# Optimization experiments

Measured on AMD Instinct MI355X. Metric: run time of the kernel, lower is better.

The kernel has to match this reference:

```python
import jax, jax.numpy as jnp
import numpy as np

D = 1024
H = 4 * D
E = 8
K = 2


def setup_inputs() -> dict:
    key = jax.random.key(0)
    ks = jax.random.split(key, 8)
    s = 1.0 / np.sqrt(D)
    sh = 1.0 / np.sqrt(H)
    return {
        "x": jax.random.normal(ks[0], (4, 2048, D), dtype=jnp.float32),
        "gate_w": jax.random.uniform(ks[1], (D, E), jnp.float32, -s, s),
        "gate_b": jax.random.uniform(ks[2], (E,), jnp.float32, -s, s),
        "w1": jax.random.uniform(ks[3], (E, D, H), jnp.float32, -s, s),
        "b1": jax.random.uniform(ks[4], (E, H), jnp.float32, -s, s),
        "w2": jax.random.uniform(ks[5], (E, H, D), jnp.float32, -sh, sh),
        "b2": jax.random.uniform(ks[6], (E, D), jnp.float32, -sh, sh),
    }


def reference(x, gate_w, gate_b, w1, b1, w2, b2):
    # Gating: softmax over experts, top-k, renormalize.
    gate_logits = jnp.einsum("bsd,de->bse", x, gate_w) + gate_b
    weights = jax.nn.softmax(gate_logits, axis=-1)
    top_w, top_idx = jax.lax.top_k(weights, K)  # [B,S,K]
    top_w = top_w / jnp.sum(top_w, axis=-1, keepdims=True)

    out = jnp.zeros_like(x)
    # Loop over the fixed, small set of experts; dense FFN per expert,
    # masked-weighted combine (same math as the per-token torch loop).
    for e in range(E):
        # combine weight for expert e per token: sum of top_w where selected
        w_e = jnp.sum(jnp.where(top_idx == e, top_w, 0.0), axis=-1)  # [B,S]
        h = jax.nn.gelu(jnp.einsum("bsd,dh->bsh", x, w1[e]) + b1[e], approximate=False)
        y = jnp.einsum("bsh,hd->bsd", h, w2[e]) + b2[e]
        out = out + w_e[..., None] * y
    return out
```

## Files before the change

### kernel.cpp

```cpp
#include <hip/hip_runtime.h>
#include <math.h>

#define T_TOK 8192
#define DDIM  1024
#define HDIM  4096
#define NEXP  8
#define BM    128
#define BN    128
#define BK    64
#define MAXROWS (T_TOK*2 + NEXP*BM)
#define MAXTILES (MAXROWS/BM)
#define KS2   2
#define NGATE (T_TOK/8)
#define NTR1  ((HDIM/64)*(DDIM/64)*NEXP)
#define NTR2  ((DDIM/64)*(HDIM/64)*NEXP)

typedef __attribute__((ext_vector_type(8))) short short8;
typedef __attribute__((ext_vector_type(4))) short short4v;
typedef __attribute__((ext_vector_type(4))) float f32x4;

typedef const __attribute__((address_space(1))) unsigned int* gp1_t;
typedef __attribute__((address_space(3))) unsigned int* lp3_t;

__device__ __forceinline__ void gld16(const void* g, void* l) {
  __builtin_amdgcn_global_load_lds((gp1_t)g, (lp3_t)l, 16, 0, 0);
}

__device__ __forceinline__ short f2bf(float f) {
  unsigned u = __float_as_uint(f);
  u += 0x7fffu + ((u >> 16) & 1u);
  return (short)(u >> 16);
}

__device__ __forceinline__ float erf_fast(float x) {
  float ax = fabsf(x);
  float t = 1.f / (1.f + 0.3275911f * ax);
  float poly = t * (0.254829592f + t * (-0.284496736f + t * (1.421413741f +
               t * (-1.453152027f + t * 1.061405429f))));
  float r = 1.f - poly * __expf(-ax * ax);
  return copysignf(r, x);
}

__device__ __forceinline__ void tr_body(float* sl ,
    const float* __restrict__ w, short* __restrict__ wt, int R, int C, int lb) {
  int ctiles = C / 64, rtiles = R / 64;
  int e  = lb / (ctiles * rtiles);
  int rm = lb % (ctiles * rtiles);
  int r0 = (rm / ctiles) * 64;
  int c0 = (rm % ctiles) * 64;
  const float* W = w + (size_t)e * R * C;
  short* O = wt + (size_t)e * R * C;
  int t = threadIdx.x;
  int lr = t >> 4, lc4 = (t & 15) * 4;
#pragma unroll
  for (int i = 0; i < 4; i++) {
    float4 v = *(const float4*)&W[(size_t)(r0 + lr + i * 16) * C + c0 + lc4];
    sl[(lr + i * 16) * 65 + lc4 + 0] = v.x;
    sl[(lr + i * 16) * 65 + lc4 + 1] = v.y;
    sl[(lr + i * 16) * 65 + lc4 + 2] = v.z;
    sl[(lr + i * 16) * 65 + lc4 + 3] = v.w;
  }
  __syncthreads();
#pragma unroll
  for (int i = 0; i < 4; i++) {
    int oc = lr + i * 16;
    short4v s;
#pragma unroll
    for (int j = 0; j < 4; j++) s[j] = f2bf(sl[(lc4 + j) * 65 + oc]);
    *(short4v*)&O[(size_t)(c0 + oc) * R + r0 + lc4] = s;
  }
}

__device__ __forceinline__ void gate_body(char* smem, int bid,
    const float* __restrict__ x, const float* __restrict__ gw,
    const float* __restrict__ gb, int2* __restrict__ toke,
    float2* __restrict__ tokw, int* __restrict__ bcnt, short* __restrict__ xb) {
  float* sg = (float*)smem;
  int* lcnt = (int*)(smem + NEXP * DDIM * 4);
  int t = threadIdx.x;
#pragma unroll
  for (int it = 0; it < 8; ++it) {
    int l0 = (it * 256 + t) * 4;
    float4 v = *(const float4*)&gw[l0];
    int d = l0 >> 3, e0 = l0 & 7;
    sg[(e0 + 0) * DDIM + d] = v.x;
    sg[(e0 + 1) * DDIM + d] = v.y;
    sg[(e0 + 2) * DDIM + d] = v.z;
    sg[(e0 + 3) * DDIM + d] = v.w;
  }
  if (t < NEXP) lcnt[t] = 0;
  __syncthreads();
  int wave = t >> 6, lane = t & 63;
  int tok0 = bid * 8 + wave * 2;
#pragma unroll
  for (int tk = 0; tk < 2; ++tk) {
    int tok = tok0 + tk;
    float p[NEXP];
#pragma unroll
    for (int e = 0; e < NEXP; e++) p[e] = 0.f;
#pragma unroll
    for (int c = 0; c < 4; c++) {
      int d = c * 256 + lane * 4;
      float4 xv = *(const float4*)&x[(size_t)tok * DDIM + d];
      short4v sv;
      sv[0] = f2bf(xv.x); sv[1] = f2bf(xv.y); sv[2] = f2bf(xv.z); sv[3] = f2bf(xv.w);
      *(short4v*)&xb[(size_t)tok * DDIM + d] = sv;
#pragma unroll
      for (int e = 0; e < NEXP; e++) {
        float4 g = *(const float4*)&sg[e * DDIM + d];
        p[e] += xv.x * g.x + xv.y * g.y + xv.z * g.z + xv.w * g.w;
      }
    }
#pragma unroll
    for (int off = 32; off; off >>= 1)
#pragma unroll
      for (int e = 0; e < NEXP; e++) p[e] += __shfl_xor(p[e], off);
    if (lane == 0) {
      float l[NEXP];
#pragma unroll
      for (int e = 0; e < NEXP; e++) l[e] = p[e] + gb[e];
      int i0 = 0;
#pragma unroll
      for (int e = 1; e < NEXP; e++) if (l[e] > l[i0]) i0 = e;
      int i1 = (i0 == 0) ? 1 : 0;
#pragma unroll
      for (int e = 0; e < NEXP; e++) if (e != i0 && l[e] > l[i1]) i1 = e;
      float ex = expf(l[i1] - l[i0]);
      float w0 = 1.f / (1.f + ex);
      toke[tok] = make_int2(i0, i1);
      tokw[tok] = make_float2(w0, 1.f - w0);
      atomicAdd(&lcnt[i0], 1);
      atomicAdd(&lcnt[i1], 1);
    }
  }
  __syncthreads();
  if (t < NEXP) bcnt[bid * NEXP + t] = lcnt[t];
}

__global__ __launch_bounds__(256) void k_front(const float* __restrict__ x,
    const float* __restrict__ gw, const float* __restrict__ gb,
    const float* __restrict__ w1, const float* __restrict__ w2,
    int2* __restrict__ toke, float2* __restrict__ tokw, int* __restrict__ bcnt,
    short* __restrict__ xb, short* __restrict__ w1t, short* __restrict__ w2t) {
  __shared__ char smem[NEXP * DDIM * 4 + 64];
  int bid = blockIdx.x;
  if (bid < NGATE) {
    gate_body(smem, bid, x, gw, gb, toke, tokw, bcnt, xb);
  } else if (bid < NGATE + NTR1) {
    tr_body((float*)smem, w1, w1t, DDIM, HDIM, bid - NGATE);
  } else {
    tr_body((float*)smem, w2, w2t, HDIM, DDIM, bid - NGATE - NTR1);
  }
}

__global__ __launch_bounds__(256) void k_plan(const int* __restrict__ bcnt,
    int* __restrict__ pbase, int* __restrict__ texp) {
  __shared__ int tot[NEXP];
  __shared__ int b[NEXP + 1];
  int t = threadIdx.x;
  if (t < NEXP) tot[t] = 0;
  __syncthreads();
  int e = t & 7, sum = 0;
  for (int i = t >> 3; i < NGATE; i += 32) sum += bcnt[i * NEXP + e];
  atomicAdd(&tot[e], sum);
  __syncthreads();
  if (t == 0) {
    b[0] = 0;
#pragma unroll
    for (int ee = 0; ee < NEXP; ee++)
      b[ee + 1] = b[ee] + ((tot[ee] + BM - 1) & ~(BM - 1));
#pragma unroll
    for (int ee = 0; ee < NEXP; ee++) pbase[ee] = b[ee];
  }
  __syncthreads();
  for (int i = t; i < MAXTILES; i += 256) {
    int r0 = i * BM, ee = -1;
#pragma unroll
    for (int k = 0; k < NEXP; k++) if (r0 >= b[k] && r0 < b[k + 1]) ee = k;
    texp[i] = ee;
  }
}

__global__ __launch_bounds__(256) void k_scatter(const int2* __restrict__ toke,
    const float2* __restrict__ tokw, const int* __restrict__ pbase,
    int* __restrict__ fill, int* __restrict__ rtok, float* __restrict__ rwgt,
    int* __restrict__ trow) {
  int tok = blockIdx.x * 256 + threadIdx.x;
  if (tok >= T_TOK) return;
  int2 te = toke[tok];
  float2 tw = tokw[tok];
  int s0 = atomicAdd(&fill[te.x], 1);
  int r0 = pbase[te.x] + s0;
  rtok[r0] = tok; rwgt[r0] = tw.x; trow[tok * 2] = r0;
  int s1 = atomicAdd(&fill[te.y], 1);
  int r1 = pbase[te.y] + s1;
  rtok[r1] = tok; rwgt[r1] = tw.y; trow[tok * 2 + 1] = r1;
}

__global__ __launch_bounds__(256) void k_out(const float* __restrict__ out2,
    const float* __restrict__ b2, const int2* __restrict__ toke,
    const float2* __restrict__ tokw, const int* __restrict__ trow,
    float* __restrict__ out) {
  int idx = blockIdx.x * 256 + threadIdx.x;
  int tok = idx >> 8;
  int seg = (idx & 255) * 4;
  int2 te = toke[tok];
  float2 tw = tokw[tok];
  int r0 = trow[tok * 2], r1 = trow[tok * 2 + 1];
  float4 a  = *(const float4*)&out2[(size_t)r0 * DDIM + seg];
  float4 c  = *(const float4*)&out2[(size_t)r1 * DDIM + seg];
  float4 p0 = *(const float4*)&b2[te.x * DDIM + seg];
  float4 p1 = *(const float4*)&b2[te.y * DDIM + seg];
  float4 o;
  o.x = tw.x * (a.x + p0.x) + tw.y * (c.x + p1.x);
  o.y = tw.x * (a.y + p0.y) + tw.y * (c.y + p1.y);
  o.z = tw.x * (a.z + p0.z) + tw.y * (c.z + p1.z);
  o.w = tw.x * (a.w + p0.w) + tw.y * (c.w + p1.w);
  *(float4*)&out[(size_t)tok * DDIM + seg] = o;
}


#define STG(ko) { \
  gld16(sA[0] + (ko), &AL[(0 * 32 + wid * 8) * BK]); \
  gld16(sA[1] + (ko), &AL[(1 * 32 + wid * 8) * BK]); \
  gld16(sA[2] + (ko), &AL[(2 * 32 + wid * 8) * BK]); \
  gld16(sA[3] + (ko), &AL[(3 * 32 + wid * 8) * BK]); \
  gld16(sB[0] + (ko), &BL[(0 * 32 + wid * 8) * BK]); \
  gld16(sB[1] + (ko), &BL[(1 * 32 + wid * 8) * BK]); \
  gld16(sB[2] + (ko), &BL[(2 * 32 + wid * 8) * BK]); \
  gld16(sB[3] + (ko), &BL[(3 * 32 + wid * 8) * BK]); }

#define MFMA_TILE { \
  __builtin_amdgcn_s_setprio(1); \
  _Pragma("unroll") \
  for (int s = 0; s < 2; ++s) { \
    int xo = ((s * 4 + kg) ^ x7) << 3; \
    short8 af[4], bg[4]; \
    _Pragma("unroll") \
    for (int i = 0; i < 4; i++) af[i] = *(short8*)&AL[(wm + i * 16 + lr) * BK + xo]; \
    _Pragma("unroll") \
    for (int j = 0; j < 4; j++) bg[j] = *(short8*)&BL[(wn + j * 16 + lr) * BK + xo]; \
    _Pragma("unroll") \
    for (int i = 0; i < 4; i++) \
    _Pragma("unroll") \
    for (int j = 0; j < 4; j++) \
      acc[i][j] = __builtin_amdgcn_mfma_f32_16x16x32_bf16(af[i], bg[j], acc[i][j], 0, 0, 0); \
  } \
  __builtin_amdgcn_s_setprio(0); }

#define GEMM_LOOP(NKv) \
  for (int kt = 0; kt < (NKv); ++kt) { \
    STG(kt * BK); \
    asm volatile("s_waitcnt vmcnt(0)" ::: "memory"); \
    __syncthreads(); \
    MFMA_TILE; \
    __syncthreads(); \
  }

__global__ __launch_bounds__(256, 4) void k_ffn1(const short* __restrict__ xb,
    const short* __restrict__ w1t, const float* __restrict__ b1,
    const int* __restrict__ rtok, const int* __restrict__ texp,
    int tile_base, short* __restrict__ hbuf) {
  int tl = blockIdx.y;
  int tm = tile_base + tl;
  int e = texp[tm];
  if (e < 0) return;
  int n0 = blockIdx.x * BN;
  const short* W = w1t + (size_t)e * HDIM * DDIM;
  __shared__ short LDSBUF[2 * BM * BK];
  short* AL = LDSBUF;
  short* BL = LDSBUF + BM * BK;
  int t = threadIdx.x, wid = t >> 6, lane = t & 63;
  int sr8 = lane >> 3, slot = lane & 7;
  int swz = (slot ^ sr8) * 8;
  const short* sA[4]; const short* sB[4];
#pragma unroll
  for (int i = 0; i < 4; i++) {
    int r = i * 32 + wid * 8 + sr8;
    int tok = rtok[tm * BM + r]; if (tok < 0) tok = 0;
    sA[i] = xb + (size_t)tok * DDIM + swz;
    sB[i] = W + (size_t)(n0 + r) * DDIM + swz;
  }

  f32x4 acc[4][4];
#pragma unroll
  for (int i = 0; i < 4; i++)
#pragma unroll
    for (int j = 0; j < 4; j++) acc[i][j] = (f32x4){0.f, 0.f, 0.f, 0.f};

  int wm = (wid >> 1) * 64, wn = (wid & 1) * 64;
  int lr = lane & 15, kg = lane >> 4, x7 = lr & 7;

  GEMM_LOOP(DDIM / BK)

  short* SB = LDSBUF + wid * (32 * 68);
#pragma unroll
  for (int p = 0; p < 2; ++p) {
#pragma unroll
    for (int i2 = 0; i2 < 2; ++i2) {
      int i = p * 2 + i2;
#pragma unroll
      for (int j = 0; j < 4; ++j) {
        int col = j * 16 + lr;
        float bias = b1[e * HDIM + n0 + wn + col];
#pragma unroll
        for (int r = 0; r < 4; ++r) {
          float v = acc[i][j][r] + bias;
          v = 0.5f * v * (1.f + erf_fast(v * 0.70710678118f));
          SB[(i2 * 16 + kg * 4 + r) * 68 + col] = f2bf(v);
        }
      }
    }
    int lrow = lane >> 1, c0 = (lane & 1) * 32;
    size_t grow = (size_t)(tl * BM + wm + p * 32 + lrow);
#pragma unroll
    for (int s = 0; s < 4; ++s) {
      short8 v = *(short8*)&SB[lrow * 68 + c0 + s * 8];
      *(short8*)&hbuf[grow * HDIM + n0 + wn + c0 + s * 8] = v;
    }
  }
}

__global__ __launch_bounds__(256, 4) void k_ffn2d(const short* __restrict__ hbuf,
    const short* __restrict__ w2t, const int* __restrict__ texp,
    int tile_base, float* __restrict__ out2) {
  int tl = blockIdx.y;
  int tm = tile_base + tl;
  int e = texp[tm];
  if (e < 0) return;
  int n0 = blockIdx.x * BN;
  const short* W = w2t + (size_t)e * DDIM * HDIM;
  __shared__ short LDSBUF[2 * BM * BK];
  short* AL = LDSBUF;
  short* BL = LDSBUF + BM * BK;
  int t = threadIdx.x, wid = t >> 6, lane = t & 63;
  int sr8 = lane >> 3, slot = lane & 7;
  int swz = (slot ^ sr8) * 8;
  const short* sA[4]; const short* sB[4];
#pragma unroll
  for (int i = 0; i < 4; i++) {
    int r = i * 32 + wid * 8 + sr8;
    sA[i] = hbuf + (size_t)(tl * BM + r) * HDIM + swz;
    sB[i] = W + (size_t)(n0 + r) * HDIM + swz;
  }

  f32x4 acc[4][4];
#pragma unroll
  for (int i = 0; i < 4; i++)
#pragma unroll
    for (int j = 0; j < 4; j++) acc[i][j] = (f32x4){0.f, 0.f, 0.f, 0.f};

  int wm = (wid >> 1) * 64, wn = (wid & 1) * 64;
  int lr = lane & 15, kg = lane >> 4, x7 = lr & 7;

  GEMM_LOOP(HDIM / BK)

  float* SBf = (float*)LDSBUF + wid * (16 * 68);
#pragma unroll
  for (int i = 0; i < 4; ++i) {
#pragma unroll
    for (int j = 0; j < 4; ++j)
#pragma unroll
      for (int r = 0; r < 4; ++r)
        SBf[(kg * 4 + r) * 68 + j * 16 + lr] = acc[i][j][r];
    int lrow = lane >> 2, c0 = (lane & 3) * 16;
    size_t grow = (size_t)(tm * BM + wm + i * 16 + lrow);
#pragma unroll
    for (int s = 0; s < 4; ++s) {
      float4 v = *(float4*)&SBf[lrow * 68 + c0 + s * 4];
      *(float4*)&out2[grow * DDIM + n0 + wn + c0 + s * 4] = v;
    }
  }
}

__global__ __launch_bounds__(256, 4) void k_ffn2a(const short* __restrict__ hbuf,
    const short* __restrict__ w2t, const float* __restrict__ b2,
    const int* __restrict__ rtok, const float* __restrict__ rwgt,
    const int* __restrict__ texp, int tile_base, float* __restrict__ out) {
  int tl = blockIdx.z;
  int tm = tile_base + tl;
  int e = texp[tm];
  if (e < 0) return;
  int kc = blockIdx.y;
  int n0 = blockIdx.x * BN;
  const short* W = w2t + (size_t)e * DDIM * HDIM;
  __shared__ short LDSBUF[2 * BM * BK];
  short* AL = LDSBUF;
  short* BL = LDSBUF + BM * BK;
  int t = threadIdx.x, wid = t >> 6, lane = t & 63;
  int sr8 = lane >> 3, slot = lane & 7;
  int swz = (slot ^ sr8) * 8;
  const int NK = HDIM / BK / KS2;
  int kbase = kc * NK * BK;
  const short* sA[4]; const short* sB[4];
#pragma unroll
  for (int i = 0; i < 4; i++) {
    int r = i * 32 + wid * 8 + sr8;
    sA[i] = hbuf + (size_t)(tl * BM + r) * HDIM + kbase + swz;
    sB[i] = W + (size_t)(n0 + r) * HDIM + kbase + swz;
  }
  f32x4 acc[4][4];
#pragma unroll
  for (int i = 0; i < 4; i++)
#pragma unroll
    for (int j = 0; j < 4; j++) acc[i][j] = (f32x4){0.f, 0.f, 0.f, 0.f};
  int wm = (wid >> 1) * 64, wn = (wid & 1) * 64;
  int lr = lane & 15, kg = lane >> 4, x7 = lr & 7;

  GEMM_LOOP(NK)

#pragma unroll
  for (int j = 0; j < 4; j++) {
    int gcol = n0 + wn + j * 16 + lr;
    float bias = (kc == 0) ? b2[e * DDIM + gcol] : 0.f;
#pragma unroll
    for (int i = 0; i < 4; i++) {
      int rl = wm + i * 16 + kg * 4;
#pragma unroll
      for (int r = 0; r < 4; r++) {
        int grow = tm * BM + rl + r;
        int tok = rtok[grow];
        if (tok >= 0) {
          float v = (acc[i][j][r] + bias) * rwgt[grow];
          atomicAdd(&out[(size_t)tok * DDIM + gcol], v);
        }
      }
    }
  }
}

extern "C" void kernel_launch(void* const* d_in, const int* in_sizes, int n_in,
                              void* d_out, int out_size, void* d_ws, size_t ws_size,
                              hipStream_t stream) {
  const float* x  = (const float*)d_in[0];
  const float* gw = (const float*)d_in[1];
  const float* gb = (const float*)d_in[2];
  const float* w1 = (const float*)d_in[3];
  const float* b1 = (const float*)d_in[4];
  const float* w2 = (const float*)d_in[5];
  const float* b2 = (const float*)d_in[6];
  float* out = (float*)d_out;
  char* ws = (char*)d_ws;

  int*    fill  = (int*)(ws + 32);
  int*    pbase = (int*)(ws + 64);
  int*    texp  = (int*)(ws + 128);
  int*    rtok  = (int*)(ws + 1024);
  float*  rwgt  = (float*)(ws + 1024 + (size_t)MAXROWS * 4);
  int2*   toke  = (int2*)(ws + 1024 + (size_t)MAXROWS * 8);
  float2* tokw  = (float2*)(ws + 1024 + (size_t)MAXROWS * 8 + (size_t)T_TOK * 8);
  int*    bcnt  = (int*)(ws + 640 * 1024);
  int*    trow  = (int*)(ws + 768 * 1024);
  size_t wbytes = (size_t)NEXP * DDIM * HDIM * 2;
  short*  w1t   = (short*)(ws + (1 << 20));
  short*  w2t   = (short*)(ws + (1 << 20) + wbytes);
  short*  xb    = (short*)(ws + (1 << 20) + 2 * wbytes);
  size_t xend   = (1 << 20) + 2 * wbytes + (size_t)T_TOK * DDIM * 2;
  size_t o2b    = (size_t)MAXROWS * DDIM * 4;
  size_t hbytes = (size_t)MAXTILES * BM * HDIM * 2;

  bool dense = ws_size >= xend + o2b + hbytes;

  hipMemsetAsync(ws, 0, 128, stream);
  hipMemsetAsync(rtok, 0xFF, (size_t)MAXROWS * 4, stream);

  k_front<<<NGATE + NTR1 + NTR2, 256, 0, stream>>>(x, gw, gb, w1, w2,
                                                   toke, tokw, bcnt, xb, w1t, w2t);
  k_plan<<<1, 256, 0, stream>>>(bcnt, pbase, texp);
  k_scatter<<<T_TOK / 256, 256, 0, stream>>>(toke, tokw, pbase, fill, rtok, rwgt, trow);

  if (dense) {
    float* out2 = (float*)(ws + xend);
    short* hbuf = (short*)(ws + xend + o2b);
    k_ffn1<<<dim3(HDIM / BN, MAXTILES), 256, 0, stream>>>(xb, w1t, b1, rtok, texp,
                                                          0, hbuf);
    k_ffn2d<<<dim3(DDIM / BN, MAXTILES), 256, 0, stream>>>(hbuf, w2t, texp, 0, out2);
    k_out<<<(T_TOK * DDIM / 4) / 256, 256, 0, stream>>>(out2, b2, toke, tokw, trow, out);
  } else {
    short* hbuf = (short*)(ws + xend);
    size_t hcap = ws_size > xend ? ws_size - xend : 0;
    int tpc = (int)(hcap / ((size_t)BM * HDIM * 2));
    if (tpc < 1) return;
    if (tpc > MAXTILES) tpc = MAXTILES;
    hipMemsetAsync(d_out, 0, (size_t)T_TOK * DDIM * 4, stream);
    for (int base = 0; base < MAXTILES; base += tpc) {
      int nt = MAXTILES - base;
      if (nt > tpc) nt = tpc;
      k_ffn1<<<dim3(HDIM / BN, nt), 256, 0, stream>>>(xb, w1t, b1, rtok, texp, base, hbuf);
      k_ffn2a<<<dim3(DDIM / BN, KS2, nt), 256, 0, stream>>>(hbuf, w2t, b2, rtok, rwgt,
                                                            texp, base, out);
    }
  }
}
```

Baseline: 588.8 us.

## Double-buffer LDS tiles with BK=32 to overlap global loads and MFMA

Halves the K tile to 32 and allocates two LDS buffers for A and B. The next tile is now prefetched with global_load_lds while the current one feeds MFMA, using a partial vmcnt wait in place of a full drain before every step. The LDS swizzle and the load-row mapping are redone for the new 32-wide rows. Total LDS per block stays the same, so occupancy is unchanged. The cost is more loop iterations and barriers per K, and only one MFMA k-step of work between syncs.

```diff
diff --git a/kernel.cpp b/kernel.cpp
--- a/kernel.cpp
+++ b/kernel.cpp
@@ -7,7 +7,7 @@
 #define NEXP  8
 #define BM    128
 #define BN    128
-#define BK    64
+#define BK    32
 #define MAXROWS (T_TOK*2 + NEXP*BM)
 #define MAXTILES (MAXROWS/BM)
 #define KS2   2
@@ -220,42 +220,51 @@
 }
 
 
-#define STG(ko) { \
-  gld16(sA[0] + (ko), &AL[(0 * 32 + wid * 8) * BK]); \
-  gld16(sA[1] + (ko), &AL[(1 * 32 + wid * 8) * BK]); \
-  gld16(sA[2] + (ko), &AL[(2 * 32 + wid * 8) * BK]); \
-  gld16(sA[3] + (ko), &AL[(3 * 32 + wid * 8) * BK]); \
-  gld16(sB[0] + (ko), &BL[(0 * 32 + wid * 8) * BK]); \
-  gld16(sB[1] + (ko), &BL[(1 * 32 + wid * 8) * BK]); \
-  gld16(sB[2] + (ko), &BL[(2 * 32 + wid * 8) * BK]); \
-  gld16(sB[3] + (ko), &BL[(3 * 32 + wid * 8) * BK]); }
-
-#define MFMA_TILE { \
+#define STG(bf, ko) { \
+  gld16(sA[0] + (ko), &AL[bf][(wid * 32 + 0) * BK]); \
+  gld16(sA[1] + (ko), &AL[bf][(wid * 32 + 16) * BK]); \
+  gld16(sB[0] + (ko), &BL[bf][(wid * 32 + 0) * BK]); \
+  gld16(sB[1] + (ko), &BL[bf][(wid * 32 + 16) * BK]); }
+
+#define MFMA_STEP(bf) { \
+  short8 af[4], bg[4]; \
+  _Pragma("unroll") \
+  for (int i = 0; i < 4; i++) af[i] = *(short8*)&AL[bf][(wm + i * 16 + lr) * BK + sph]; \
+  _Pragma("unroll") \
+  for (int j = 0; j < 4; j++) bg[j] = *(short8*)&BL[bf][(wn + j * 16 + lr) * BK + sph]; \
   __builtin_amdgcn_s_setprio(1); \
   _Pragma("unroll") \
-  for (int s = 0; s < 2; ++s) { \
-    int xo = ((s * 4 + kg) ^ x7) << 3; \
-    short8 af[4], bg[4]; \
-    _Pragma("unroll") \
-    for (int i = 0; i < 4; i++) af[i] = *(short8*)&AL[(wm + i * 16 + lr) * BK + xo]; \
-    _Pragma("unroll") \
-    for (int j = 0; j < 4; j++) bg[j] = *(short8*)&BL[(wn + j * 16 + lr) * BK + xo]; \
-    _Pragma("unroll") \
-    for (int i = 0; i < 4; i++) \
-    _Pragma("unroll") \
-    for (int j = 0; j < 4; j++) \
-      acc[i][j] = __builtin_amdgcn_mfma_f32_16x16x32_bf16(af[i], bg[j], acc[i][j], 0, 0, 0); \
-  } \
+  for (int i = 0; i < 4; i++) \
+  _Pragma("unroll") \
+  for (int j = 0; j < 4; j++) \
+    acc[i][j] = __builtin_amdgcn_mfma_f32_16x16x32_bf16(af[i], bg[j], acc[i][j], 0, 0, 0); \
   __builtin_amdgcn_s_setprio(0); }
 
 #define GEMM_LOOP(NKv) \
+  STG(0, 0); \
   for (int kt = 0; kt < (NKv); ++kt) { \
-    STG(kt * BK); \
-    asm volatile("s_waitcnt vmcnt(0)" ::: "memory"); \
-    __syncthreads(); \
-    MFMA_TILE; \
-    __syncthreads(); \
-  }
+    int cur = kt & 1; \
+    if (kt + 1 < (NKv)) { \
+      STG(cur ^ 1, (kt + 1) * BK); \
+      asm volatile("s_waitcnt vmcnt(4)" ::: "memory"); \
+    } else { \
+      asm volatile("s_waitcnt vmcnt(0)" ::: "memory"); \
+    } \
+    __builtin_amdgcn_s_barrier(); \
+    __builtin_amdgcn_sched_barrier(0); \
+    MFMA_STEP(cur); \
+    __builtin_amdgcn_sched_barrier(0); \
+    __builtin_amdgcn_s_barrier(); \
+    __builtin_amdgcn_sched_barrier(0); \
+  }
+
+#define GEMM_IDX \
+  int t = threadIdx.x, wid = t >> 6, lane = t & 63; \
+  int srow = lane >> 2;                                \
+  int sgsl = ((lane & 3) ^ ((lane >> 2) & 3) ^ ((lane >> 4) & 3)) * 8;  \
+  int wm = (wid >> 1) * 64, wn = (wid & 1) * 64; \
+  int lr = lane & 15, kg = lane >> 4; \
+  int sph = ((kg ^ (lr & 3) ^ ((lr >> 2) & 3))) * 8;
 
 __global__ __launch_bounds__(256, 4) void k_ffn1(const short* __restrict__ xb,
     const short* __restrict__ w1t, const float* __restrict__ b1,
@@ -267,19 +276,16 @@
   if (e < 0) return;
   int n0 = blockIdx.x * BN;
   const short* W = w1t + (size_t)e * HDIM * DDIM;
-  __shared__ short LDSBUF[2 * BM * BK];
-  short* AL = LDSBUF;
-  short* BL = LDSBUF + BM * BK;
-  int t = threadIdx.x, wid = t >> 6, lane = t & 63;
-  int sr8 = lane >> 3, slot = lane & 7;
-  int swz = (slot ^ sr8) * 8;
-  const short* sA[4]; const short* sB[4];
-#pragma unroll
-  for (int i = 0; i < 4; i++) {
-    int r = i * 32 + wid * 8 + sr8;
+  __shared__ short AL[2][BM * BK];
+  __shared__ short BL[2][BM * BK];
+  GEMM_IDX
+  const short* sA[2]; const short* sB[2];
+#pragma unroll
+  for (int i = 0; i < 2; i++) {
+    int r = wid * 32 + i * 16 + srow;
     int tok = rtok[tm * BM + r]; if (tok < 0) tok = 0;
-    sA[i] = xb + (size_t)tok * DDIM + swz;
-    sB[i] = W + (size_t)(n0 + r) * DDIM + swz;
+    sA[i] = xb + (size_t)tok * DDIM + sgsl;
+    sB[i] = W + (size_t)(n0 + r) * DDIM + sgsl;
   }
 
   f32x4 acc[4][4];
@@ -288,12 +294,9 @@
 #pragma unroll
     for (int j = 0; j < 4; j++) acc[i][j] = (f32x4){0.f, 0.f, 0.f, 0.f};
 
-  int wm = (wid >> 1) * 64, wn = (wid & 1) * 64;
-  int lr = lane & 15, kg = lane >> 4, x7 = lr & 7;
-
   GEMM_LOOP(DDIM / BK)
 
-  short* SB = LDSBUF + wid * (32 * 68);
+  short* SB = (short*)AL + wid * (32 * 68);
 #pragma unroll
   for (int p = 0; p < 2; ++p) {
 #pragma unroll
@@ -330,18 +333,15 @@
   if (e < 0) return;
   int n0 = blockIdx.x * BN;
   const short* W = w2t + (size_t)e * DDIM * HDIM;
-  __shared__ short LDSBUF[2 * BM * BK];
-  short* AL = LDSBUF;
-  short* BL = LDSBUF + BM * BK;
-  int t = threadIdx.x, wid = t >> 6, lane = t & 63;
-  int sr8 = lane >> 3, slot = lane & 7;
-  int swz = (slot ^ sr8) * 8;
-  const short* sA[4]; const short* sB[4];
-#pragma unroll
-  for (int i = 0; i < 4; i++) {
-    int r = i * 32 + wid * 8 + sr8;
-    sA[i] = hbuf + (size_t)(tl * BM + r) * HDIM + swz;
-    sB[i] = W + (size_t)(n0 + r) * HDIM + swz;
+  __shared__ short AL[2][BM * BK];
+  __shared__ short BL[2][BM * BK];
+  GEMM_IDX
+  const short* sA[2]; const short* sB[2];
+#pragma unroll
+  for (int i = 0; i < 2; i++) {
+    int r = wid * 32 + i * 16 + srow;
+    sA[i] = hbuf + (size_t)(tl * BM + r) * HDIM + sgsl;
+    sB[i] = W + (size_t)(n0 + r) * HDIM + sgsl;
   }
 
   f32x4 acc[4][4];
@@ -350,12 +350,9 @@
 #pragma unroll
     for (int j = 0; j < 4; j++) acc[i][j] = (f32x4){0.f, 0.f, 0.f, 0.f};
 
-  int wm = (wid >> 1) * 64, wn = (wid & 1) * 64;
-  int lr = lane & 15, kg = lane >> 4, x7 = lr & 7;
-
   GEMM_LOOP(HDIM / BK)
 
-  float* SBf = (float*)LDSBUF + wid * (16 * 68);
+  float* SBf = (float*)AL + wid * (16 * 68);
 #pragma unroll
   for (int i = 0; i < 4; ++i) {
 #pragma unroll
@@ -384,28 +381,23 @@
   int kc = blockIdx.y;
   int n0 = blockIdx.x * BN;
   const short* W = w2t + (size_t)e * DDIM * HDIM;
-  __shared__ short LDSBUF[2 * BM * BK];
-  short* AL = LDSBUF;
-  short* BL = LDSBUF + BM * BK;
-  int t = threadIdx.x, wid = t >> 6, lane = t & 63;
-  int sr8 = lane >> 3, slot = lane & 7;
-  int swz = (slot ^ sr8) * 8;
+  __shared__ short AL[2][BM * BK];
+  __shared__ short BL[2][BM * BK];
+  GEMM_IDX
   const int NK = HDIM / BK / KS2;
   int kbase = kc * NK * BK;
-  const short* sA[4]; const short* sB[4];
-#pragma unroll
-  for (int i = 0; i < 4; i++) {
-    int r = i * 32 + wid * 8 + sr8;
-    sA[i] = hbuf + (size_t)(tl * BM + r) * HDIM + kbase + swz;
-    sB[i] = W + (size_t)(n0 + r) * HDIM + kbase + swz;
+  const short* sA[2]; const short* sB[2];
+#pragma unroll
+  for (int i = 0; i < 2; i++) {
+    int r = wid * 32 + i * 16 + srow;
+    sA[i] = hbuf + (size_t)(tl * BM + r) * HDIM + kbase + sgsl;
+    sB[i] = W + (size_t)(n0 + r) * HDIM + kbase + sgsl;
   }
   f32x4 acc[4][4];
 #pragma unroll
   for (int i = 0; i < 4; i++)
 #pragma unroll
     for (int j = 0; j < 4; j++) acc[i][j] = (f32x4){0.f, 0.f, 0.f, 0.f};
-  int wm = (wid >> 1) * 64, wn = (wid & 1) * 64;
-  int lr = lane & 15, kg = lane >> 4, x7 = lr & 7;
 
   GEMM_LOOP(NK)
 
```

Result: slower. 669.3 us (+13.7%).
